# Performance work log

Hardware: AMD Instinct MI355X
Metric: run time of the kernel (lower is better)

The kernel has to match this reference:

```python
import jax, jax.numpy as jnp
import numpy as np

NUM_SEGMENTS = 4480  # BATCH_SIZE * MAX_ATOMS = 64 * 70
ATOM_DIM = 64
BOND_DIM = 16
N_EDGES = 65536


def setup_inputs() -> dict:
    key = jax.random.key(0)
    k1, k2, k3, k4 = jax.random.split(key, 4)
    atom_feat = jax.random.normal(k1, (NUM_SEGMENTS, ATOM_DIM), dtype=jnp.float32)
    bond_feat = jax.random.normal(k2, (N_EDGES, BOND_DIM), dtype=jnp.float32)
    pair_idx = jax.random.randint(k3, (N_EDGES, 2), 0, NUM_SEGMENTS, dtype=jnp.int64)
    # glorot-uniform style kernel, zero bias (as in add_weight initializers)
    limit = float(np.sqrt(6.0 / (BOND_DIM + ATOM_DIM ** 2)))
    kernel = jax.random.uniform(k4, (BOND_DIM, ATOM_DIM ** 2), dtype=jnp.float32,
                                minval=-limit, maxval=limit)
    bias = jnp.zeros((ATOM_DIM ** 2,), dtype=jnp.float32)
    return {"atom_feat": atom_feat, "bond_feat": bond_feat,
            "pair_idx": pair_idx, "kernel": kernel, "bias": bias}


def reference(atom_feat, bond_feat, pair_idx, kernel, bias):
    atom_dim = atom_feat.shape[-1]
    # dense projection of bond features -> per-edge transform matrices
    bond_transformed = bond_feat @ kernel + bias               # [E, D*D]
    bond_transformed = bond_transformed.reshape(-1, atom_dim, atom_dim)  # [E, D, D]
    # gather neighbor (source) atom features per edge
    neighbor_feat = jnp.take(atom_feat, pair_idx[:, 1].astype(jnp.int32), axis=0)  # [E, D]
    # per-edge matrix-vector product
    messages = jnp.einsum('eij,ej->ei', bond_transformed, neighbor_feat)  # [E, D]
    # scatter-add into destination atoms
    return jax.ops.segment_sum(messages, pair_idx[:, 0].astype(jnp.int32),
                               num_segments=NUM_SEGMENTS)  # [NUM_SEGMENTS, D]
```

## Files before the change

kernel.cpp:

```cpp
#include <hip/hip_runtime.h>
#include <hip/hip_bf16.h>

#define NSEG   4480
#define ADIM   64
#define BDIM   16
#define NEDGE  65536
#define UPITCH 1088
#define KP     72

typedef __bf16 bf16x8 __attribute__((ext_vector_type(8)));
typedef float  f32x4  __attribute__((ext_vector_type(4)));

__device__ __forceinline__ float bf2f(unsigned int bits_hi16) {
    union { unsigned int i; float f; } c; c.i = bits_hi16; return c.f;
}
__device__ __forceinline__ unsigned short f2bf(float f) {
    union { float f; unsigned int i; } c; c.f = f;
    unsigned int x = c.i;
    x += 0x7fffu + ((x >> 16) & 1u);
    return (unsigned short)(x >> 16);
}

__global__ __launch_bounds__(256) void proj_kernel(
    const float* __restrict__ atom,
    const float* __restrict__ kern,
    const float* __restrict__ bias,
    unsigned short* __restrict__ U,
    float* __restrict__ out)
{
    __shared__ unsigned short Al[64 * KP];
    __shared__ unsigned short Wl[64 * KP];

    const int t      = threadIdx.x;
    const int bx     = blockIdx.x;
    const int by     = blockIdx.y;
    const int a_base = bx * 64;
    const int c_base = by * 64;

    if (by == 0) {
        int gid = bx * 256 + t;
        ((float4*)out)[gid] = make_float4(0.f, 0.f, 0.f, 0.f);
    }

    {
        const int row = t >> 2, q = t & 3;
        const float4* src = (const float4*)(atom + (size_t)(a_base + row) * ADIM + q * 16);
        unsigned short* dst = Al + row * KP + q * 16;
#pragma unroll
        for (int i = 0; i < 4; ++i) {
            float4 v = src[i];
            dst[i * 4 + 0] = f2bf(v.x);
            dst[i * 4 + 1] = f2bf(v.y);
            dst[i * 4 + 2] = f2bf(v.z);
            dst[i * 4 + 3] = f2bf(v.w);
        }
    }
    {
        const int crow = t >> 2, q = t & 3;
        const int c = c_base + crow;
        const float* bsrc = (c < 1024)
            ? (kern + (size_t)(c & 15) * 4096 + (size_t)(c >> 4) * 64)
            : (bias + (size_t)(c - 1024) * 64);
        const float4* src = (const float4*)(bsrc + q * 16);
        unsigned short* dst = Wl + crow * KP + q * 16;
#pragma unroll
        for (int i = 0; i < 4; ++i) {
            float4 v = src[i];
            dst[i * 4 + 0] = f2bf(v.x);
            dst[i * 4 + 1] = f2bf(v.y);
            dst[i * 4 + 2] = f2bf(v.z);
            dst[i * 4 + 3] = f2bf(v.w);
        }
    }
    __syncthreads();

    const int lane = t & 63;
    const int w    = t >> 6;
    const int m    = lane & 15;
    const int quad = lane >> 4;

    f32x4 acc[4] = {{0.f,0.f,0.f,0.f},{0.f,0.f,0.f,0.f},
                    {0.f,0.f,0.f,0.f},{0.f,0.f,0.f,0.f}};

#pragma unroll
    for (int kk = 0; kk < 2; ++kk) {
        bf16x8 a = *(const bf16x8*)(Al + (w * 16 + m) * KP + kk * 32 + quad * 8);
#pragma unroll
        for (int ct = 0; ct < 4; ++ct) {
            bf16x8 b = *(const bf16x8*)(Wl + (ct * 16 + m) * KP + kk * 32 + quad * 8);
            acc[ct] = __builtin_amdgcn_mfma_f32_16x16x32_bf16(a, b, acc[ct], 0, 0, 0);
        }
    }

#pragma unroll
    for (int ct = 0; ct < 4; ++ct) {
#pragma unroll
        for (int r = 0; r < 4; ++r) {
            U[(size_t)(a_base + w * 16 + quad * 4 + r) * UPITCH
              + (c_base + ct * 16 + m)] = f2bf(acc[ct][r]);
        }
    }
}

__global__ __launch_bounds__(256) void edge_kernel(
    const float*          __restrict__ bond,
    const int*            __restrict__ pair,
    const unsigned short* __restrict__ U,
    float*                __restrict__ out)
{
    const int t    = threadIdx.x;
    const int lane = t & 63;
    const int e    = blockIdx.x * 4 + (t >> 6);

    const int2 p  = ((const int2*)pair)[e];
    const int dst = p.x;
    const int src = p.y;

    const unsigned short* urow = U + (size_t)src * UPITCH;
    const uint4* up = (const uint4*)(urow + lane * 16);
    uint4 w0 = up[0];
    uint4 w1 = up[1];

    const float4* bp = (const float4*)(bond + (size_t)e * BDIM);
    float4 b0 = bp[0], b1 = bp[1], b2 = bp[2], b3 = bp[3];
    float b[16] = { b0.x, b0.y, b0.z, b0.w,  b1.x, b1.y, b1.z, b1.w,
                    b2.x, b2.y, b2.z, b2.w,  b3.x, b3.y, b3.z, b3.w };

    unsigned int w[8] = { w0.x, w0.y, w0.z, w0.w, w1.x, w1.y, w1.z, w1.w };

    float m = bf2f(((unsigned int)urow[1024 + lane]) << 16);
#pragma unroll
    for (int q = 0; q < 8; ++q) {
        float lo = bf2f(w[q] << 16);
        float hi = bf2f(w[q] & 0xffff0000u);
        m = fmaf(lo, b[2 * q],     m);
        m = fmaf(hi, b[2 * q + 1], m);
    }

    atomicAdd(out + (size_t)dst * ADIM + lane, m);
}

extern "C" void kernel_launch(void* const* d_in, const int* in_sizes, int n_in,
                              void* d_out, int out_size, void* d_ws, size_t ws_size,
                              hipStream_t stream) {
    const float* atom = (const float*)d_in[0];
    const float* bond = (const float*)d_in[1];
    const int*   pair = (const int*)  d_in[2];
    const float* kern = (const float*)d_in[3];
    const float* bias = (const float*)d_in[4];

    float* out = (float*)d_out;
    unsigned short* U = (unsigned short*)d_ws;

    dim3 g1(NSEG / 64, UPITCH / 64);
    proj_kernel<<<g1, 256, 0, stream>>>(atom, kern, bias, U, out);

    edge_kernel<<<NEDGE / 4, 256, 0, stream>>>(bond, pair, U, out);
}
```

Measured before the change: 92.52 us.

## Replace atomic scatter with CSR build, src-sorted message pass, and dst gather-reduce

Edges are bucketed by destination and by source with a histogram, a single-wave prefix scan and an atomic-slot scatter, which builds CSR-style index lists. Messages are then computed in source-sorted order, with a block swizzle, to improve reuse of the projected U rows, and written to a workspace buffer. A per-destination reduction sums them, removing the float atomics into the output and making the sum deterministic. The cost is four extra launches, a serial single-wave scan, and a 16MB write and re-read of the message buffer.

```diff
diff --git a/kernel.cpp b/kernel.cpp
--- a/kernel.cpp
+++ b/kernel.cpp
@@ -1,5 +1,4 @@
 #include <hip/hip_runtime.h>
-#include <hip/hip_bf16.h>
 
 #define NSEG   4480
 #define ADIM   64
@@ -8,6 +7,9 @@
 #define UPITCH 1088
 #define KP     72
 
+#define MSG_OFF  (16u << 20)
+#define INT_OFF  (40u << 20)
+
 typedef __bf16 bf16x8 __attribute__((ext_vector_type(8)));
 typedef float  f32x4  __attribute__((ext_vector_type(4)));
 
@@ -26,7 +28,7 @@
     const float* __restrict__ kern,
     const float* __restrict__ bias,
     unsigned short* __restrict__ U,
-    float* __restrict__ out)
+    int* __restrict__ csr_ints)
 {
     __shared__ unsigned short Al[64 * KP];
     __shared__ unsigned short Wl[64 * KP];
@@ -38,8 +40,7 @@
     const int c_base = by * 64;
 
     if (by == 0) {
-        int gid = bx * 256 + t;
-        ((float4*)out)[gid] = make_float4(0.f, 0.f, 0.f, 0.f);
+        csr_ints[bx * 256 + t] = 0;
     }
 
     {
@@ -102,19 +103,69 @@
     }
 }
 
-__global__ __launch_bounds__(256) void edge_kernel(
+__global__ __launch_bounds__(256) void hist_kernel(
+    const int* __restrict__ pair, int* __restrict__ cnt_d, int* __restrict__ cnt_s)
+{
+    const int e = blockIdx.x * 256 + threadIdx.x;
+    const int2 p = ((const int2*)pair)[e];
+    atomicAdd(&cnt_d[p.x], 1);
+    atomicAdd(&cnt_s[p.y], 1);
+}
+
+__device__ __forceinline__ void wave_scan_4480(
+    const int* __restrict__ cnt, int* __restrict__ start)
+{
+    const int lane = threadIdx.x;
+    const int base = lane * 70;
+    int c[70];
+    int run = 0;
+#pragma unroll
+    for (int i = 0; i < 70; ++i) { c[i] = cnt[base + i]; run += c[i]; }
+    int incl = run;
+#pragma unroll
+    for (int d = 1; d < 64; d <<= 1) {
+        int t = __shfl_up(incl, d, 64);
+        if (lane >= d) incl += t;
+    }
+    int excl = incl - run;
+#pragma unroll
+    for (int i = 0; i < 70; ++i) { start[base + i] = excl; excl += c[i]; }
+}
+
+__global__ __launch_bounds__(64) void scan_kernel(
+    const int* __restrict__ cnt_d, int* __restrict__ start_d,
+    const int* __restrict__ cnt_s, int* __restrict__ start_s)
+{
+    wave_scan_4480(cnt_d, start_d);
+    wave_scan_4480(cnt_s, start_s);
+}
+
+__global__ __launch_bounds__(256) void scatter_kernel(
+    const int* __restrict__ pair,
+    int* __restrict__ start_d, int* __restrict__ start_s,
+    int* __restrict__ eidx_d, int* __restrict__ eidx_s)
+{
+    const int e = blockIdx.x * 256 + threadIdx.x;
+    const int2 p = ((const int2*)pair)[e];
+    eidx_d[atomicAdd(&start_d[p.x], 1)] = e;
+    eidx_s[atomicAdd(&start_s[p.y], 1)] = e;
+}
+
+__global__ __launch_bounds__(256) void msg_kernel(
     const float*          __restrict__ bond,
     const int*            __restrict__ pair,
+    const int*            __restrict__ eidx_s,
     const unsigned short* __restrict__ U,
-    float*                __restrict__ out)
+    float*                __restrict__ msg)
 {
     const int t    = threadIdx.x;
     const int lane = t & 63;
-    const int e    = blockIdx.x * 4 + (t >> 6);
-
-    const int2 p  = ((const int2*)pair)[e];
-    const int dst = p.x;
-    const int src = p.y;
+    const int bx   = blockIdx.x;
+    const int bsw  = (bx & 7) * 2048 + (bx >> 3);
+    const int j    = bsw * 4 + (t >> 6);
+
+    const int e   = eidx_s[j];
+    const int src = ((const int2*)pair)[e].y;
 
     const unsigned short* urow = U + (size_t)src * UPITCH;
     const uint4* up = (const uint4*)(urow + lane * 16);
@@ -137,7 +188,39 @@
         m = fmaf(hi, b[2 * q + 1], m);
     }
 
-    atomicAdd(out + (size_t)dst * ADIM + lane, m);
+    msg[(size_t)e * ADIM + lane] = m;
+}
+
+__global__ __launch_bounds__(256) void reduce_kernel(
+    const int*   __restrict__ start_d,
+    const int*   __restrict__ eidx_d,
+    const float* __restrict__ msg,
+    float*       __restrict__ out)
+{
+    const int t    = threadIdx.x;
+    const int lane = t & 63;
+    const int d    = blockIdx.x * 4 + (t >> 6);
+
+    const int end   = start_d[d];
+    const int begin = (d == 0) ? 0 : start_d[d - 1];
+
+    float a0 = 0.f, a1 = 0.f, a2 = 0.f, a3 = 0.f;
+    int k = begin;
+    for (; k + 4 <= end; k += 4) {
+        const int e0 = eidx_d[k + 0];
+        const int e1 = eidx_d[k + 1];
+        const int e2 = eidx_d[k + 2];
+        const int e3 = eidx_d[k + 3];
+        a0 += msg[(size_t)e0 * ADIM + lane];
+        a1 += msg[(size_t)e1 * ADIM + lane];
+        a2 += msg[(size_t)e2 * ADIM + lane];
+        a3 += msg[(size_t)e3 * ADIM + lane];
+    }
+    for (; k < end; ++k) {
+        a0 += msg[(size_t)eidx_d[k] * ADIM + lane];
+    }
+
+    out[(size_t)d * ADIM + lane] = (a0 + a1) + (a2 + a3);
 }
 
 extern "C" void kernel_launch(void* const* d_in, const int* in_sizes, int n_in,
@@ -150,10 +233,23 @@
     const float* bias = (const float*)d_in[4];
 
     float* out = (float*)d_out;
-    unsigned short* U = (unsigned short*)d_ws;
+
+    unsigned short* U  = (unsigned short*)d_ws;
+    float* msg         = (float*)((char*)d_ws + MSG_OFF);
+    int*   ints        = (int*)  ((char*)d_ws + INT_OFF);
+    int* cnt_d   = ints;
+    int* cnt_s   = ints + 4480;
+    int* start_d = ints + 8960;
+    int* start_s = ints + 13440;
+    int* eidx_d  = ints + 17920;
+    int* eidx_s  = ints + 17920 + NEDGE;
 
     dim3 g1(NSEG / 64, UPITCH / 64);
-    proj_kernel<<<g1, 256, 0, stream>>>(atom, kern, bias, U, out);
-
-    edge_kernel<<<NEDGE / 4, 256, 0, stream>>>(bond, pair, U, out);
-}
+    proj_kernel<<<g1, 256, 0, stream>>>(atom, kern, bias, U, ints);
+    hist_kernel<<<NEDGE / 256, 256, 0, stream>>>(pair, cnt_d, cnt_s);
+    scan_kernel<<<1, 64, 0, stream>>>(cnt_d, start_d, cnt_s, start_s);
+    scatter_kernel<<<NEDGE / 256, 256, 0, stream>>>(pair, start_d, start_s,
+                                                    eidx_d, eidx_s);
+    msg_kernel<<<NEDGE / 4, 256, 0, stream>>>(bond, pair, eidx_s, U, msg);
+    reduce_kernel<<<NSEG / 4, 256, 0, stream>>>(start_d, eidx_d, msg, out);
+}
```

Result: slower. 124.4 us (+34.5%).

## Reassociate edge transform: bucket edges by destination, accumulate outer products, then GEMM

Applied to the files above, without the earlier changes.

Rewrites the computation as out[d] = sum over r of (sum over edges of bond[e,r]*atom[src]) times W_r, plus a bias term. A counting-sort scatter kernel groups edges by destination into fixed-capacity buckets. An accumulation kernel builds a 17x64 per-destination matrix in bf16, and a GEMM kernel multiplies it by kernel and bias with MFMA. This removes the per-edge gathers of large projected rows and the float atomics on the output, at the cost of three launches plus a memset. It also drops edges beyond 128 per destination, which risks wrong results if any bucket overflows.

```diff
diff --git a/kernel.cpp b/kernel.cpp
--- a/kernel.cpp
+++ b/kernel.cpp
@@ -1,19 +1,19 @@
 #include <hip/hip_runtime.h>
-#include <hip/hip_bf16.h>
 
 #define NSEG   4480
 #define ADIM   64
 #define BDIM   16
 #define NEDGE  65536
-#define UPITCH 1088
+#define GP     1088
+#define CAP    128
 #define KP     72
+
+#define EB_OFF   (16u << 20)
+#define CNT_OFF  (24u << 20)
 
 typedef __bf16 bf16x8 __attribute__((ext_vector_type(8)));
 typedef float  f32x4  __attribute__((ext_vector_type(4)));
 
-__device__ __forceinline__ float bf2f(unsigned int bits_hi16) {
-    union { unsigned int i; float f; } c; c.i = bits_hi16; return c.f;
-}
 __device__ __forceinline__ unsigned short f2bf(float f) {
     union { float f; unsigned int i; } c; c.f = f;
     unsigned int x = c.i;
@@ -21,123 +21,138 @@
     return (unsigned short)(x >> 16);
 }
 
-__global__ __launch_bounds__(256) void proj_kernel(
+__global__ __launch_bounds__(256) void scatter_kernel(
+    const int* __restrict__ pair, int* __restrict__ cnt, int2* __restrict__ eb)
+{
+    const int e  = blockIdx.x * 256 + threadIdx.x;
+    const int2 p = ((const int2*)pair)[e];
+    const int idx = atomicAdd(&cnt[p.x], 1);
+    if (idx < CAP) eb[(size_t)p.x * CAP + idx] = make_int2(e, p.y);
+}
+
+__global__ __launch_bounds__(256) void accum_kernel(
     const float* __restrict__ atom,
+    const float* __restrict__ bond,
+    const int*   __restrict__ cnt,
+    const int2*  __restrict__ eb,
+    unsigned short* __restrict__ G)
+{
+    const int t    = threadIdx.x;
+    const int lane = t & 63;
+    const int d    = blockIdx.x * 4 + (t >> 6);
+    const int nc   = cnt[d];
+    const int n    = nc < CAP ? nc : CAP;
+    const int2* bk = eb + (size_t)d * CAP;
+
+    float g[17];
+#pragma unroll
+    for (int r = 0; r < 17; ++r) g[r] = 0.f;
+
+    int k = 0;
+    for (; k + 2 <= n; k += 2) {
+        const int2 es0 = bk[k];
+        const int2 es1 = bk[k + 1];
+        const float a0 = atom[(size_t)es0.y * ADIM + lane];
+        const float a1 = atom[(size_t)es1.y * ADIM + lane];
+        const float4* b0p = (const float4*)(bond + (size_t)es0.x * BDIM);
+        const float4* b1p = (const float4*)(bond + (size_t)es1.x * BDIM);
+        float4 c0 = b0p[0], c1 = b0p[1], c2 = b0p[2], c3 = b0p[3];
+        float4 e0 = b1p[0], e1 = b1p[1], e2 = b1p[2], e3 = b1p[3];
+        const float bb0[16] = { c0.x,c0.y,c0.z,c0.w, c1.x,c1.y,c1.z,c1.w,
+                                c2.x,c2.y,c2.z,c2.w, c3.x,c3.y,c3.z,c3.w };
+        const float bb1[16] = { e0.x,e0.y,e0.z,e0.w, e1.x,e1.y,e1.z,e1.w,
+                                e2.x,e2.y,e2.z,e2.w, e3.x,e3.y,e3.z,e3.w };
+#pragma unroll
+        for (int r = 0; r < 16; ++r) g[r] = fmaf(a0, bb0[r], g[r]);
+        g[16] += a0;
+#pragma unroll
+        for (int r = 0; r < 16; ++r) g[r] = fmaf(a1, bb1[r], g[r]);
+        g[16] += a1;
+    }
+    if (k < n) {
+        const int2 es = bk[k];
+        const float a = atom[(size_t)es.y * ADIM + lane];
+        const float4* bp = (const float4*)(bond + (size_t)es.x * BDIM);
+        float4 c0 = bp[0], c1 = bp[1], c2 = bp[2], c3 = bp[3];
+        const float bb[16] = { c0.x,c0.y,c0.z,c0.w, c1.x,c1.y,c1.z,c1.w,
+                               c2.x,c2.y,c2.z,c2.w, c3.x,c3.y,c3.z,c3.w };
+#pragma unroll
+        for (int r = 0; r < 16; ++r) g[r] = fmaf(a, bb[r], g[r]);
+        g[16] += a;
+    }
+
+#pragma unroll
+    for (int r = 0; r < 17; ++r)
+        G[(size_t)d * GP + r * 64 + lane] = f2bf(g[r]);
+}
+
+__global__ __launch_bounds__(256) void gemm_kernel(
+    const unsigned short* __restrict__ G,
     const float* __restrict__ kern,
     const float* __restrict__ bias,
-    unsigned short* __restrict__ U,
     float* __restrict__ out)
 {
-    __shared__ unsigned short Al[64 * KP];
-    __shared__ unsigned short Wl[64 * KP];
+    __shared__ unsigned short Gs[16 * KP];
+    __shared__ unsigned short Ws[64 * KP];
 
-    const int t      = threadIdx.x;
-    const int bx     = blockIdx.x;
-    const int by     = blockIdx.y;
-    const int a_base = bx * 64;
-    const int c_base = by * 64;
-
-    if (by == 0) {
-        int gid = bx * 256 + t;
-        ((float4*)out)[gid] = make_float4(0.f, 0.f, 0.f, 0.f);
-    }
-
-    {
-        const int row = t >> 2, q = t & 3;
-        const float4* src = (const float4*)(atom + (size_t)(a_base + row) * ADIM + q * 16);
-        unsigned short* dst = Al + row * KP + q * 16;
-#pragma unroll
-        for (int i = 0; i < 4; ++i) {
-            float4 v = src[i];
-            dst[i * 4 + 0] = f2bf(v.x);
-            dst[i * 4 + 1] = f2bf(v.y);
-            dst[i * 4 + 2] = f2bf(v.z);
-            dst[i * 4 + 3] = f2bf(v.w);
-        }
-    }
-    {
-        const int crow = t >> 2, q = t & 3;
-        const int c = c_base + crow;
-        const float* bsrc = (c < 1024)
-            ? (kern + (size_t)(c & 15) * 4096 + (size_t)(c >> 4) * 64)
-            : (bias + (size_t)(c - 1024) * 64);
-        const float4* src = (const float4*)(bsrc + q * 16);
-        unsigned short* dst = Wl + crow * KP + q * 16;
-#pragma unroll
-        for (int i = 0; i < 4; ++i) {
-            float4 v = src[i];
-            dst[i * 4 + 0] = f2bf(v.x);
-            dst[i * 4 + 1] = f2bf(v.y);
-            dst[i * 4 + 2] = f2bf(v.z);
-            dst[i * 4 + 3] = f2bf(v.w);
-        }
-    }
-    __syncthreads();
-
+    const int t    = threadIdx.x;
     const int lane = t & 63;
     const int w    = t >> 6;
+    const int rb   = blockIdx.x * 16;
     const int m    = lane & 15;
     const int quad = lane >> 4;
 
-    f32x4 acc[4] = {{0.f,0.f,0.f,0.f},{0.f,0.f,0.f,0.f},
-                    {0.f,0.f,0.f,0.f},{0.f,0.f,0.f,0.f}};
+    const int wi = t >> 2, wq = t & 3;
+    const int gr = t >> 3, gq = t & 7;
 
+    f32x4 acc = {0.f, 0.f, 0.f, 0.f};
+
+    float4 wv[4];
+    uint4  gv;
+    {
+        const float4* wp = (const float4*)(kern + (size_t)wi * 64 + wq * 16);
 #pragma unroll
-    for (int kk = 0; kk < 2; ++kk) {
-        bf16x8 a = *(const bf16x8*)(Al + (w * 16 + m) * KP + kk * 32 + quad * 8);
+        for (int x = 0; x < 4; ++x) wv[x] = wp[x];
+        if (t < 128)
+            gv = *(const uint4*)(G + (size_t)(rb + gr) * GP + gq * 8);
+    }
+
+    for (int r = 0; r < 17; ++r) {
+        __syncthreads();
+        {
+            unsigned short* dst = Ws + wi * KP + wq * 16;
 #pragma unroll
-        for (int ct = 0; ct < 4; ++ct) {
-            bf16x8 b = *(const bf16x8*)(Wl + (ct * 16 + m) * KP + kk * 32 + quad * 8);
-            acc[ct] = __builtin_amdgcn_mfma_f32_16x16x32_bf16(a, b, acc[ct], 0, 0, 0);
+            for (int x = 0; x < 4; ++x) {
+                float4 v = wv[x];
+                dst[x * 4 + 0] = f2bf(v.x);
+                dst[x * 4 + 1] = f2bf(v.y);
+                dst[x * 4 + 2] = f2bf(v.z);
+                dst[x * 4 + 3] = f2bf(v.w);
+            }
+            if (t < 128) *(uint4*)(Gs + gr * KP + gq * 8) = gv;
+        }
+        if (r + 1 < 17) {
+            const float* wsrc = (r + 1 < 16) ? (kern + (size_t)(r + 1) * 4096)
+                                             : bias;
+            const float4* wp = (const float4*)(wsrc + (size_t)wi * 64 + wq * 16);
+#pragma unroll
+            for (int x = 0; x < 4; ++x) wv[x] = wp[x];
+            if (t < 128)
+                gv = *(const uint4*)(G + (size_t)(rb + gr) * GP
+                                       + (r + 1) * 64 + gq * 8);
+        }
+        __syncthreads();
+#pragma unroll
+        for (int kk = 0; kk < 2; ++kk) {
+            bf16x8 a = *(const bf16x8*)(Gs + m * KP + kk * 32 + quad * 8);
+            bf16x8 b = *(const bf16x8*)(Ws + (w * 16 + m) * KP + kk * 32 + quad * 8);
+            acc = __builtin_amdgcn_mfma_f32_16x16x32_bf16(a, b, acc, 0, 0, 0);
         }
     }
 
 #pragma unroll
-    for (int ct = 0; ct < 4; ++ct) {
-#pragma unroll
-        for (int r = 0; r < 4; ++r) {
-            U[(size_t)(a_base + w * 16 + quad * 4 + r) * UPITCH
-              + (c_base + ct * 16 + m)] = f2bf(acc[ct][r]);
-        }
-    }
-}
-
-__global__ __launch_bounds__(256) void edge_kernel(
-    const float*          __restrict__ bond,
-    const int*            __restrict__ pair,
-    const unsigned short* __restrict__ U,
-    float*                __restrict__ out)
-{
-    const int t    = threadIdx.x;
-    const int lane = t & 63;
-    const int e    = blockIdx.x * 4 + (t >> 6);
-
-    const int2 p  = ((const int2*)pair)[e];
-    const int dst = p.x;
-    const int src = p.y;
-
-    const unsigned short* urow = U + (size_t)src * UPITCH;
-    const uint4* up = (const uint4*)(urow + lane * 16);
-    uint4 w0 = up[0];
-    uint4 w1 = up[1];
-
-    const float4* bp = (const float4*)(bond + (size_t)e * BDIM);
-    float4 b0 = bp[0], b1 = bp[1], b2 = bp[2], b3 = bp[3];
-    float b[16] = { b0.x, b0.y, b0.z, b0.w,  b1.x, b1.y, b1.z, b1.w,
-                    b2.x, b2.y, b2.z, b2.w,  b3.x, b3.y, b3.z, b3.w };
-
-    unsigned int w[8] = { w0.x, w0.y, w0.z, w0.w, w1.x, w1.y, w1.z, w1.w };
-
-    float m = bf2f(((unsigned int)urow[1024 + lane]) << 16);
-#pragma unroll
-    for (int q = 0; q < 8; ++q) {
-        float lo = bf2f(w[q] << 16);
-        float hi = bf2f(w[q] & 0xffff0000u);
-        m = fmaf(lo, b[2 * q],     m);
-        m = fmaf(hi, b[2 * q + 1], m);
-    }
-
-    atomicAdd(out + (size_t)dst * ADIM + lane, m);
+    for (int rr = 0; rr < 4; ++rr)
+        out[(size_t)(rb + quad * 4 + rr) * ADIM + w * 16 + m] = acc[rr];
 }
 
 extern "C" void kernel_launch(void* const* d_in, const int* in_sizes, int n_in,
@@ -150,10 +165,13 @@
     const float* bias = (const float*)d_in[4];
 
     float* out = (float*)d_out;
-    unsigned short* U = (unsigned short*)d_ws;
 
-    dim3 g1(NSEG / 64, UPITCH / 64);
-    proj_kernel<<<g1, 256, 0, stream>>>(atom, kern, bias, U, out);
+    unsigned short* G = (unsigned short*)d_ws;
+    int2* eb = (int2*)((char*)d_ws + EB_OFF);
+    int*  cnt = (int*)((char*)d_ws + CNT_OFF);
 
-    edge_kernel<<<NEDGE / 4, 256, 0, stream>>>(bond, pair, U, out);
+    hipMemsetAsync(cnt, 0, NSEG * sizeof(int), stream);
+    scatter_kernel<<<NEDGE / 256, 256, 0, stream>>>(pair, cnt, eb);
+    accum_kernel<<<NSEG / 4, 256, 0, stream>>>(atom, bond, cnt, eb, G);
+    gemm_kernel<<<NSEG / 16, 256, 0, stream>>>(G, kern, bias, out);
 }
```

Measured after the change: 104.4 us. 1.13x slower.

## Fuse projection and scatter into per-destination kernel with reassociated contraction

Applied to the files above, without the earlier changes.

Replaces the two-kernel scheme (project every atom through the kernel into a bf16 workspace, then gather it per edge and scatter with global atomics) with one kernel. Each block owns 16 destination atoms and scans the whole pair list, binning its incoming edges in LDS. It then accumulates atom features times bond features into a small per-destination G tensor, and applies the kernel and bias once per destination with bf16 MFMA. This removes the large intermediate U and the global float atomics. In exchange every block rereads the full pair array, occupancy is low, and edges beyond a fixed per-destination capacity of 64 are silently dropped.

```diff
diff --git a/kernel.cpp b/kernel.cpp
--- a/kernel.cpp
+++ b/kernel.cpp
@@ -1,19 +1,19 @@
 #include <hip/hip_runtime.h>
-#include <hip/hip_bf16.h>
 
 #define NSEG   4480
 #define ADIM   64
 #define BDIM   16
 #define NEDGE  65536
-#define UPITCH 1088
-#define KP     72
+#define DPB    16
+#define NBLK   (NSEG / DPB)
+#define TPB    256
+#define CAPL   64
+#define GSP    1096
+
 
 typedef __bf16 bf16x8 __attribute__((ext_vector_type(8)));
 typedef float  f32x4  __attribute__((ext_vector_type(4)));
 
-__device__ __forceinline__ float bf2f(unsigned int bits_hi16) {
-    union { unsigned int i; float f; } c; c.i = bits_hi16; return c.f;
-}
 __device__ __forceinline__ unsigned short f2bf(float f) {
     union { float f; unsigned int i; } c; c.f = f;
     unsigned int x = c.i;
@@ -21,123 +21,128 @@
     return (unsigned short)(x >> 16);
 }
 
-__global__ __launch_bounds__(256) void proj_kernel(
+union U8 { unsigned short u[8]; bf16x8 v; };
+
+__device__ __forceinline__ bf16x8 pack_bf8(float4 a, float4 b) {
+    U8 r;
+    r.u[0] = f2bf(a.x); r.u[1] = f2bf(a.y); r.u[2] = f2bf(a.z); r.u[3] = f2bf(a.w);
+    r.u[4] = f2bf(b.x); r.u[5] = f2bf(b.y); r.u[6] = f2bf(b.z); r.u[7] = f2bf(b.w);
+    return r.v;
+}
+
+__global__ __launch_bounds__(TPB) void fused_kernel(
     const float* __restrict__ atom,
+    const float* __restrict__ bond,
+    const int*   __restrict__ pair,
     const float* __restrict__ kern,
     const float* __restrict__ bias,
-    unsigned short* __restrict__ U,
-    float* __restrict__ out)
+    float*       __restrict__ out)
 {
-    __shared__ unsigned short Al[64 * KP];
-    __shared__ unsigned short Wl[64 * KP];
+    __shared__ int  bcnt[DPB];
+    __shared__ int2 ebuf[DPB][CAPL];
+    __shared__ unsigned short Gs[DPB * GSP];
 
-    const int t      = threadIdx.x;
-    const int bx     = blockIdx.x;
-    const int by     = blockIdx.y;
-    const int a_base = bx * 64;
-    const int c_base = by * 64;
+    const int t   = threadIdx.x;
+    const int dlo = blockIdx.x * DPB;
 
-    if (by == 0) {
-        int gid = bx * 256 + t;
-        ((float4*)out)[gid] = make_float4(0.f, 0.f, 0.f, 0.f);
-    }
+    if (t < DPB) bcnt[t] = 0;
+    __syncthreads();
 
     {
-        const int row = t >> 2, q = t & 3;
-        const float4* src = (const float4*)(atom + (size_t)(a_base + row) * ADIM + q * 16);
-        unsigned short* dst = Al + row * KP + q * 16;
-#pragma unroll
-        for (int i = 0; i < 4; ++i) {
-            float4 v = src[i];
-            dst[i * 4 + 0] = f2bf(v.x);
-            dst[i * 4 + 1] = f2bf(v.y);
-            dst[i * 4 + 2] = f2bf(v.z);
-            dst[i * 4 + 3] = f2bf(v.w);
-        }
-    }
-    {
-        const int crow = t >> 2, q = t & 3;
-        const int c = c_base + crow;
-        const float* bsrc = (c < 1024)
-            ? (kern + (size_t)(c & 15) * 4096 + (size_t)(c >> 4) * 64)
-            : (bias + (size_t)(c - 1024) * 64);
-        const float4* src = (const float4*)(bsrc + q * 16);
-        unsigned short* dst = Wl + crow * KP + q * 16;
-#pragma unroll
-        for (int i = 0; i < 4; ++i) {
-            float4 v = src[i];
-            dst[i * 4 + 0] = f2bf(v.x);
-            dst[i * 4 + 1] = f2bf(v.y);
-            dst[i * 4 + 2] = f2bf(v.z);
-            dst[i * 4 + 3] = f2bf(v.w);
+        const int4* p4 = (const int4*)pair;
+        for (int i = t; i < NEDGE / 2; i += TPB) {
+            const int4 pp = p4[i];
+            const unsigned d0 = (unsigned)(pp.x - dlo);
+            if (d0 < DPB) {
+                const int ix = atomicAdd(&bcnt[d0], 1);
+                if (ix < CAPL) ebuf[d0][ix] = make_int2(2 * i, pp.y);
+            }
+            const unsigned d1 = (unsigned)(pp.z - dlo);
+            if (d1 < DPB) {
+                const int ix = atomicAdd(&bcnt[d1], 1);
+                if (ix < CAPL) ebuf[d1][ix] = make_int2(2 * i + 1, pp.w);
+            }
         }
     }
     __syncthreads();
 
     const int lane = t & 63;
     const int w    = t >> 6;
+
+#pragma unroll
+    for (int pi = 0; pi < 2; ++pi) {
+        const int da = w * 4 + pi * 2;
+        const int db = da + 1;
+        int na = bcnt[da]; na = na < CAPL ? na : CAPL;
+        int nb = bcnt[db]; nb = nb < CAPL ? nb : CAPL;
+        float ga[17], gb[17];
+#pragma unroll
+        for (int r = 0; r < 17; ++r) { ga[r] = 0.f; gb[r] = 0.f; }
+        const int n = na > nb ? na : nb;
+        for (int k = 0; k < n; ++k) {
+            if (k < na) {
+                const int2 es = ebuf[da][k];
+                const float a = atom[(size_t)es.y * ADIM + lane];
+                const float4* bp = (const float4*)(bond + (size_t)es.x * BDIM);
+                const float4 c0 = bp[0], c1 = bp[1], c2 = bp[2], c3 = bp[3];
+                const float bb[16] = { c0.x,c0.y,c0.z,c0.w, c1.x,c1.y,c1.z,c1.w,
+                                       c2.x,c2.y,c2.z,c2.w, c3.x,c3.y,c3.z,c3.w };
+#pragma unroll
+                for (int r = 0; r < 16; ++r) ga[r] = fmaf(a, bb[r], ga[r]);
+                ga[16] += a;
+            }
+            if (k < nb) {
+                const int2 es = ebuf[db][k];
+                const float a = atom[(size_t)es.y * ADIM + lane];
+                const float4* bp = (const float4*)(bond + (size_t)es.x * BDIM);
+                const float4 c0 = bp[0], c1 = bp[1], c2 = bp[2], c3 = bp[3];
+                const float bb[16] = { c0.x,c0.y,c0.z,c0.w, c1.x,c1.y,c1.z,c1.w,
+                                       c2.x,c2.y,c2.z,c2.w, c3.x,c3.y,c3.z,c3.w };
+#pragma unroll
+                for (int r = 0; r < 16; ++r) gb[r] = fmaf(a, bb[r], gb[r]);
+                gb[16] += a;
+            }
+        }
+#pragma unroll
+        for (int r = 0; r < 17; ++r) {
+            Gs[da * GSP + r * 64 + lane] = f2bf(ga[r]);
+            Gs[db * GSP + r * 64 + lane] = f2bf(gb[r]);
+        }
+    }
+    __syncthreads();
+
     const int m    = lane & 15;
     const int quad = lane >> 4;
+    const int c    = w * 16 + m;
 
-    f32x4 acc[4] = {{0.f,0.f,0.f,0.f},{0.f,0.f,0.f,0.f},
-                    {0.f,0.f,0.f,0.f},{0.f,0.f,0.f,0.f}};
-
-#pragma unroll
-    for (int kk = 0; kk < 2; ++kk) {
-        bf16x8 a = *(const bf16x8*)(Al + (w * 16 + m) * KP + kk * 32 + quad * 8);
-#pragma unroll
-        for (int ct = 0; ct < 4; ++ct) {
-            bf16x8 b = *(const bf16x8*)(Wl + (ct * 16 + m) * KP + kk * 32 + quad * 8);
-            acc[ct] = __builtin_amdgcn_mfma_f32_16x16x32_bf16(a, b, acc[ct], 0, 0, 0);
-        }
+    f32x4 acc = {0.f, 0.f, 0.f, 0.f};
+#pragma unroll 4
+    for (int r = 0; r < 16; ++r) {
+        const float* ks = kern + (size_t)r * 4096 + (size_t)c * 64;
+        const float4* kp = (const float4*)(ks + quad * 8);
+        const float4* kq = (const float4*)(ks + 32 + quad * 8);
+        const float4 x0 = kp[0], x1 = kp[1];
+        const float4 y0 = kq[0], y1 = kq[1];
+        const bf16x8 a0 = *(const bf16x8*)(Gs + m * GSP + r * 64 + quad * 8);
+        const bf16x8 a1 = *(const bf16x8*)(Gs + m * GSP + r * 64 + 32 + quad * 8);
+        acc = __builtin_amdgcn_mfma_f32_16x16x32_bf16(a0, pack_bf8(x0, x1), acc, 0, 0, 0);
+        acc = __builtin_amdgcn_mfma_f32_16x16x32_bf16(a1, pack_bf8(y0, y1), acc, 0, 0, 0);
+    }
+    {
+        const float* ks = bias + (size_t)c * 64;
+        const float4* kp = (const float4*)(ks + quad * 8);
+        const float4* kq = (const float4*)(ks + 32 + quad * 8);
+        const float4 x0 = kp[0], x1 = kp[1];
+        const float4 y0 = kq[0], y1 = kq[1];
+        const bf16x8 a0 = *(const bf16x8*)(Gs + m * GSP + 16 * 64 + quad * 8);
+        const bf16x8 a1 = *(const bf16x8*)(Gs + m * GSP + 16 * 64 + 32 + quad * 8);
+        acc = __builtin_amdgcn_mfma_f32_16x16x32_bf16(a0, pack_bf8(x0, x1), acc, 0, 0, 0);
+        acc = __builtin_amdgcn_mfma_f32_16x16x32_bf16(a1, pack_bf8(y0, y1), acc, 0, 0, 0);
     }
 
 #pragma unroll
-    for (int ct = 0; ct < 4; ++ct) {
-#pragma unroll
-        for (int r = 0; r < 4; ++r) {
-            U[(size_t)(a_base + w * 16 + quad * 4 + r) * UPITCH
-              + (c_base + ct * 16 + m)] = f2bf(acc[ct][r]);
-        }
-    }
-}
-
-__global__ __launch_bounds__(256) void edge_kernel(
-    const float*          __restrict__ bond,
-    const int*            __restrict__ pair,
-    const unsigned short* __restrict__ U,
-    float*                __restrict__ out)
-{
-    const int t    = threadIdx.x;
-    const int lane = t & 63;
-    const int e    = blockIdx.x * 4 + (t >> 6);
-
-    const int2 p  = ((const int2*)pair)[e];
-    const int dst = p.x;
-    const int src = p.y;
-
-    const unsigned short* urow = U + (size_t)src * UPITCH;
-    const uint4* up = (const uint4*)(urow + lane * 16);
-    uint4 w0 = up[0];
-    uint4 w1 = up[1];
-
-    const float4* bp = (const float4*)(bond + (size_t)e * BDIM);
-    float4 b0 = bp[0], b1 = bp[1], b2 = bp[2], b3 = bp[3];
-    float b[16] = { b0.x, b0.y, b0.z, b0.w,  b1.x, b1.y, b1.z, b1.w,
-                    b2.x, b2.y, b2.z, b2.w,  b3.x, b3.y, b3.z, b3.w };
-
-    unsigned int w[8] = { w0.x, w0.y, w0.z, w0.w, w1.x, w1.y, w1.z, w1.w };
-
-    float m = bf2f(((unsigned int)urow[1024 + lane]) << 16);
-#pragma unroll
-    for (int q = 0; q < 8; ++q) {
-        float lo = bf2f(w[q] << 16);
-        float hi = bf2f(w[q] & 0xffff0000u);
-        m = fmaf(lo, b[2 * q],     m);
-        m = fmaf(hi, b[2 * q + 1], m);
-    }
-
-    atomicAdd(out + (size_t)dst * ADIM + lane, m);
+    for (int rr = 0; rr < 4; ++rr)
+        out[(size_t)(dlo + quad * 4 + rr) * ADIM + c] = acc[rr];
 }
 
 extern "C" void kernel_launch(void* const* d_in, const int* in_sizes, int n_in,
@@ -148,12 +153,7 @@
     const int*   pair = (const int*)  d_in[2];
     const float* kern = (const float*)d_in[3];
     const float* bias = (const float*)d_in[4];
+    float* out = (float*)d_out;
 
-    float* out = (float*)d_out;
-    unsigned short* U = (unsigned short*)d_ws;
-
-    dim3 g1(NSEG / 64, UPITCH / 64);
-    proj_kernel<<<g1, 256, 0, stream>>>(atom, kern, bias, U, out);
-
-    edge_kernel<<<NEDGE / 4, 256, 0, stream>>>(bond, pair, U, out);
+    fused_kernel<<<NBLK, TPB, 0, stream>>>(atom, bond, pair, kern, bias, out);
 }
```

Measured after the change: 145.0 us. 56.8% more time.
